# Performance work log

Hardware: AMD Instinct MI355X
Metric: run time of the kernel (lower is better)

Reference implementation:

```python
import jax, jax.numpy as jnp
import numpy as np

N_NODES = 100000


def _gcn_conv(x, W, b, src, dst, n_nodes):
    # PyG GCNConv: linear transform, then symmetric-normalized sum aggregation.
    h = x @ W  # [N, out]
    deg = jax.ops.segment_sum(jnp.ones_like(dst, dtype=h.dtype), dst, num_segments=n_nodes)
    dis = jnp.where(deg > 0, jax.lax.rsqrt(jnp.maximum(deg, 1.0)), 0.0)  # deg^-1/2
    norm = dis[src] * dis[dst]  # [E]
    msg = h[src] * norm[:, None]  # gather + scale
    out = jax.ops.segment_sum(msg, dst, num_segments=n_nodes)  # scatter-add at dst
    return out + b


def setup_inputs() -> dict:
    key = jax.random.key(0)
    k1, k2, k3, k4, k5, k6 = jax.random.split(key, 6)
    F_IN, HID, OUT = 128, 16, 2
    E = 3200000
    x = jax.random.normal(k1, (N_NODES, F_IN), dtype=jnp.float32)
    edge_index = jax.random.randint(k2, (2, E), 0, N_NODES, dtype=jnp.int64)
    W1 = jax.random.normal(k3, (F_IN, HID), dtype=jnp.float32) * (1.0 / np.sqrt(F_IN))
    b1 = jnp.zeros((HID,), dtype=jnp.float32)
    W2 = jax.random.normal(k4, (HID, OUT), dtype=jnp.float32) * (1.0 / np.sqrt(HID))
    b2 = jnp.zeros((OUT,), dtype=jnp.float32)
    return {"x": x, "edge_index": edge_index, "W1": W1, "b1": b1, "W2": W2, "b2": b2}


def reference(x, edge_index, W1, b1, W2, b2):
    n = x.shape[0]
    # add self-loops (PyG default add_self_loops=True, same edges for both layers)
    loops = jnp.arange(n, dtype=edge_index.dtype)
    src = jnp.concatenate([edge_index[0], loops])
    dst = jnp.concatenate([edge_index[1], loops])
    h = _gcn_conv(x, W1, b1, src, dst, n)
    h = jax.nn.relu(h)
    h = _gcn_conv(h, W2, b2, src, dst, n)
    return jax.nn.log_softmax(h, axis=1)
```

## Files before the change

### kernel.cpp

```cpp
#include <hip/hip_runtime.h>
#include <math.h>

#define FIN 128
#define HID 16
#define CH 8192
#define BSH 7
#define BNODES 128
#define LSH 25
#define SRCM 0x1FFFFFFu
#define SORTCAP 8192
#define BCAP 5120


__device__ __forceinline__ float bf2f(unsigned int bits16) {
    return __uint_as_float(bits16 << 16);
}
__device__ __forceinline__ unsigned short f2bf(float f) {
    unsigned int u = __float_as_uint(f);
    return (unsigned short)((u + 0x7FFFu + ((u >> 16) & 1u)) >> 16);
}

__device__ __forceinline__ int blockScan1024(int v, int* w16) {
    int lane = threadIdx.x & 63, wid = threadIdx.x >> 6;
#pragma unroll
    for (int off = 1; off < 64; off <<= 1) {
        int u = __shfl_up(v, off, 64);
        if (lane >= off) v += u;
    }
    if (lane == 63) w16[wid] = v;
    __syncthreads();
    if (wid == 0) {
        int w = (lane < 16) ? w16[lane] : 0;
#pragma unroll
        for (int off = 1; off < 16; off <<= 1) {
            int u = __shfl_up(w, off, 64);
            if (lane >= off) w += u;
        }
        if (lane < 16) w16[lane] = w;
    }
    __syncthreads();
    return v + ((wid > 0) ? w16[wid - 1] : 0);
}

__global__ void k_detect(const unsigned int* __restrict__ ew, int* __restrict__ flag) {
    __shared__ int nz;
    if (threadIdx.x == 0) nz = 0;
    __syncthreads();
    if (ew[2 * threadIdx.x + 1] != 0u) nz = 1;
    __syncthreads();
    if (threadIdx.x == 0) *flag = (nz == 0) ? 1 : 0;
}

__global__ __launch_bounds__(1024) void k_scatC(
    const void* __restrict__ ei, const int* __restrict__ flag,
    unsigned int* __restrict__ rec, int* __restrict__ runstart,
    int E, int NB) {
    __shared__ int h[1024];
    __shared__ int cur[1024];
    __shared__ int w16[16];
    __shared__ unsigned int outr[CH];
    int c = blockIdx.x, t = threadIdx.x;
    int e0 = c * CH;
    int ecnt = min(CH, E - e0);
    bool f = (*flag != 0);
    h[t] = 0;
    __syncthreads();
    for (int i = t; i < ecnt; i += 1024) {
        int d = f ? (int)((const long long*)ei)[E + e0 + i] : ((const int*)ei)[E + e0 + i];
        atomicAdd(&h[d >> BSH], 1);
    }
    __syncthreads();
    int v = h[t];
    int incl = blockScan1024(v, w16);
    int excl = incl - v;
    if (t < NB) {
        cur[t] = excl;
        runstart[(size_t)c * (NB + 1) + t] = excl;
    }
    if (t == 0) runstart[(size_t)c * (NB + 1) + NB] = ecnt;
    __syncthreads();
    for (int i = t; i < ecnt; i += 1024) {
        int ss, d;
        if (f) { const long long* p = (const long long*)ei; ss = (int)p[e0 + i]; d = (int)p[E + e0 + i]; }
        else   { const int* p = (const int*)ei;             ss = p[e0 + i];      d = p[E + e0 + i]; }
        int pos = atomicAdd(&cur[d >> BSH], 1);
        outr[pos] = ((unsigned int)(d & (BNODES - 1)) << LSH) | (unsigned int)ss;
    }
    __syncthreads();
    for (int i = t; i < ecnt; i += 1024)
        rec[e0 + i] = outr[i];
}

__global__ __launch_bounds__(1024) void k_sort2F(
    const unsigned int* __restrict__ rec, const int* __restrict__ runstart,
    unsigned int* __restrict__ rec2, int* __restrict__ row_ptr,
    int* __restrict__ cnt, int NB, int NC, int n) {
    __shared__ unsigned int stg[SORTCAP];
    __shared__ int w16[16];
    __shared__ int offA[512], lenA[512], baseA[512];
    __shared__ int h[BNODES], hs[BNODES], curq[BNODES];
    __shared__ int Ltot;
    int b = blockIdx.x, t = threadIdx.x;
    int l = 0, sbase = 0;
    if (t < NC) {
        const int* rs = runstart + (size_t)t * (NB + 1);
        int a = rs[b];
        l = rs[b + 1] - a;
        sbase = t * CH + a;
    }
    int incl = blockScan1024(l, w16);
    if (t < NC) { offA[t] = incl - l; lenA[t] = l; baseA[t] = sbase; }
    if (t < BNODES) h[t] = 0;
    if (t == 1023) Ltot = incl;
    __syncthreads();
    int L = min(Ltot, SORTCAP);
    int grp = t >> 4, lane16 = t & 15;
    for (int c = grp; c < NC; c += 64) {
        int off = offA[c], len = lenA[c], sb = baseA[c];
        for (int j = lane16; j < len; j += 16) {
            if (off + j < SORTCAP) {
                unsigned int r = rec[sb + j];
                stg[off + j] = r;
                atomicAdd(&h[r >> LSH], 1);
            }
        }
    }
    __syncthreads();
    int hv = (t < BNODES) ? h[t] : 0;
    if (t < BNODES) hs[t] = hv;
    __syncthreads();
    for (int off = 1; off < BNODES; off <<= 1) {
        int u = (t < BNODES && t >= off) ? hs[t - off] : 0;
        __syncthreads();
        if (t < BNODES) hs[t] += u;
        __syncthreads();
    }
    int bb = b * BCAP;
    if (t < BNODES) {
        int excl = hs[t] - hv;
        curq[t] = excl;
        int node = (b << BSH) + t;
        if (node < n) { row_ptr[node] = bb + excl; cnt[node] = hv; }
    }
    __syncthreads();
    for (int j = t; j < L; j += 1024) {
        unsigned int r = stg[j];
        int pos = atomicAdd(&curq[r >> LSH], 1);
        if (pos < BCAP) rec2[bb + pos] = r & SRCM;
    }
}

__global__ __launch_bounds__(256) void k_gemm1(
    const float* __restrict__ x, const float* __restrict__ W1,
    const int* __restrict__ cnt, unsigned short* __restrict__ g1b, int n) {
    __shared__ float sW[FIN][HID];
    for (int t = threadIdx.x; t < FIN * HID; t += 256) sW[t / HID][t % HID] = W1[t];
    __syncthreads();
    int i = blockIdx.x * 256 + threadIdx.x;
    if (i >= n) return;
    const float4* xr = (const float4*)(x + (size_t)i * FIN);
    float acc[HID];
#pragma unroll
    for (int c = 0; c < HID; ++c) acc[c] = 0.f;
    for (int k4 = 0; k4 < FIN / 4; ++k4) {
        float4 v = xr[k4];
#pragma unroll
        for (int c = 0; c < HID; ++c)
            acc[c] += v.x * sW[4*k4][c] + v.y * sW[4*k4+1][c]
                    + v.z * sW[4*k4+2][c] + v.w * sW[4*k4+3][c];
    }
    float di = rsqrtf((float)cnt[i] + 1.0f);
    unsigned int pk[8];
#pragma unroll
    for (int q = 0; q < 8; ++q) {
        unsigned int lo = f2bf(acc[2*q] * di);
        unsigned int hi = f2bf(acc[2*q+1] * di);
        pk[q] = lo | (hi << 16);
    }
    uint4* rp = (uint4*)(g1b + (size_t)i * HID);
    uint4 w0 = {pk[0], pk[1], pk[2], pk[3]};
    uint4 w1 = {pk[4], pk[5], pk[6], pk[7]};
    rp[0] = w0; rp[1] = w1;
}

__global__ __launch_bounds__(256) void k_agg1F(
    const int* __restrict__ row_ptr, const int* __restrict__ cnt,
    const unsigned int* __restrict__ rec2, const unsigned short* __restrict__ g1b,
    const float* __restrict__ b1, const float* __restrict__ W2,
    float* __restrict__ g2, int n) {
    int tid = blockIdx.x * 256 + threadIdx.x;
    int node = tid >> 2, q = tid & 3;
    if (node >= n) return;
    int r0 = row_ptr[node], r1 = r0 + cnt[node];
    const uint2* gp = (const uint2*)g1b;
    float a0 = 0.f, a1 = 0.f, a2 = 0.f, a3 = 0.f;
    int j = r0;
    for (; j + 3 < r1; j += 4) {
        unsigned int s0 = rec2[j], s1 = rec2[j+1], s2 = rec2[j+2], s3 = rec2[j+3];
        uint2 u0 = gp[(size_t)s0 * 4 + q];
        uint2 u1 = gp[(size_t)s1 * 4 + q];
        uint2 u2 = gp[(size_t)s2 * 4 + q];
        uint2 u3 = gp[(size_t)s3 * 4 + q];
        a0 += bf2f(u0.x & 0xFFFFu); a1 += bf2f(u0.x >> 16);
        a2 += bf2f(u0.y & 0xFFFFu); a3 += bf2f(u0.y >> 16);
        a0 += bf2f(u1.x & 0xFFFFu); a1 += bf2f(u1.x >> 16);
        a2 += bf2f(u1.y & 0xFFFFu); a3 += bf2f(u1.y >> 16);
        a0 += bf2f(u2.x & 0xFFFFu); a1 += bf2f(u2.x >> 16);
        a2 += bf2f(u2.y & 0xFFFFu); a3 += bf2f(u2.y >> 16);
        a0 += bf2f(u3.x & 0xFFFFu); a1 += bf2f(u3.x >> 16);
        a2 += bf2f(u3.y & 0xFFFFu); a3 += bf2f(u3.y >> 16);
    }
    for (; j < r1; ++j) {
        uint2 u = gp[(size_t)rec2[j] * 4 + q];
        a0 += bf2f(u.x & 0xFFFFu); a1 += bf2f(u.x >> 16);
        a2 += bf2f(u.y & 0xFFFFu); a3 += bf2f(u.y >> 16);
    }
    uint2 us = gp[(size_t)node * 4 + q];
    a0 += bf2f(us.x & 0xFFFFu); a1 += bf2f(us.x >> 16);
    a2 += bf2f(us.y & 0xFFFFu); a3 += bf2f(us.y >> 16);
    float di = rsqrtf((float)(r1 - r0) + 1.0f);
    int c4 = q << 2;
    float av[4] = {a0, a1, a2, a3};
    float h0 = 0.f, h1 = 0.f;
#pragma unroll
    for (int k = 0; k < 4; ++k) {
        int ch = c4 + k;
        float r = fmaxf(av[k] * di + b1[ch], 0.f);
        h0 += r * W2[ch * 2 + 0];
        h1 += r * W2[ch * 2 + 1];
    }
    h0 += __shfl_xor(h0, 1); h0 += __shfl_xor(h0, 2);
    h1 += __shfl_xor(h1, 1); h1 += __shfl_xor(h1, 2);
    if (q == 0) {
        float2 g; g.x = h0 * di; g.y = h1 * di;
        *(float2*)(g2 + 2 * (size_t)node) = g;
    }
}

__global__ __launch_bounds__(256) void k_aggB(
    const int* __restrict__ row_ptr, const int* __restrict__ cnt,
    const unsigned int* __restrict__ rec2, const float* __restrict__ g2,
    const float* __restrict__ b2, float* __restrict__ out, int n) {
    int tid = blockIdx.x * 256 + threadIdx.x;
    int node = tid >> 1, c = tid & 1;
    if (node >= n) return;
    int r0 = row_ptr[node], r1 = r0 + cnt[node];
    float a0 = 0.f, a1 = 0.f, a2 = 0.f, a3 = 0.f;
    int j = r0;
    for (; j + 3 < r1; j += 4) {
        unsigned int s0 = rec2[j], s1 = rec2[j+1], s2 = rec2[j+2], s3 = rec2[j+3];
        a0 += g2[2 * (size_t)s0 + c];
        a1 += g2[2 * (size_t)s1 + c];
        a2 += g2[2 * (size_t)s2 + c];
        a3 += g2[2 * (size_t)s3 + c];
    }
    for (; j < r1; ++j) a0 += g2[2 * (size_t)rec2[j] + c];
    float acc = (a0 + a1) + (a2 + a3);
    acc += g2[2 * (size_t)node + c];
    float di = rsqrtf((float)(r1 - r0) + 1.0f);
    float z  = acc * di + b2[c];
    float zo = __shfl_xor(z, 1);
    float mx = fmaxf(z, zo);
    float l  = mx + logf(expf(z - mx) + expf(zo - mx));
    out[2 * (size_t)node + c] = z - l;
}

extern "C" void kernel_launch(void* const* d_in, const int* in_sizes, int n_in,
                              void* d_out, int out_size, void* d_ws, size_t ws_size,
                              hipStream_t stream) {
    const float* x  = (const float*)d_in[0];
    const void*  ei = d_in[1];
    const float* W1 = (const float*)d_in[2];
    const float* b1 = (const float*)d_in[3];
    const float* W2 = (const float*)d_in[4];
    const float* b2 = (const float*)d_in[5];
    float* out = (float*)d_out;

    const int N = in_sizes[0] / FIN;
    const int E = in_sizes[1] / 2;

    const int NB = (N + BNODES - 1) >> BSH;
    const int NC = (E + CH - 1) / CH;

    char* w = (char*)d_ws;
    auto carve = [&](size_t bytes) { char* p = w; w += (bytes + 255) / 256 * 256; return p; };
    int*            flag     = (int*)carve(256);
    int*            runstart = (int*)carve((size_t)NC * (NB + 1) * 4);
    unsigned int*   rec      = (unsigned int*)carve((size_t)E * 4);
    unsigned int*   rec2     = (unsigned int*)carve((size_t)NB * BCAP * 4);
    int*            row_ptr  = (int*)carve((size_t)N * 4);
    int*            cnt      = (int*)carve((size_t)N * 4);
    unsigned short* g1b      = (unsigned short*)carve((size_t)N * HID * 2);
    float*          g2       = (float*)carve((size_t)N * 2 * 4);

    const int nbN = (N + 255) / 256;

    k_detect<<<1, 128, 0, stream>>>((const unsigned int*)ei, flag);
    k_scatC<<<NC, 1024, 0, stream>>>(ei, flag, rec, runstart, E, NB);
    k_sort2F<<<NB, 1024, 0, stream>>>(rec, runstart, rec2, row_ptr, cnt, NB, NC, N);
    k_gemm1<<<nbN, 256, 0, stream>>>(x, W1, cnt, g1b, N);
    k_agg1F<<<(N * 4 + 255) / 256, 256, 0, stream>>>(row_ptr, cnt, rec2, g1b, b1, W2, g2, N);
    k_aggB<<<(N * 2 + 255) / 256, 256, 0, stream>>>(row_ptr, cnt, rec2, g2, b2, out, N);
}
```

Measured before the change: 210.2 us.

## Fuse dtype detection, register-cache edges, nontemporal streams, widen aggregation threads

The separate dtype-detect kernel is folded into the scatter kernel. The scatter kernel now loads each edge's src and dst once into registers and reuses them, where it previously read the edge list twice. Streaming buffers use nontemporal loads and stores so they do not pollute the cache. The layer-1 aggregation moves from 4 to 2 threads per node with 16-byte gathers, and layer 2 uses one thread per node with 8-way unrolled float2 gathers. The changes cut launches, global reads and shuffles, but use more registers per thread and leave fewer threads to hide gather latency.

```diff
diff --git a/kernel.cpp b/kernel.cpp
--- a/kernel.cpp
+++ b/kernel.cpp
@@ -42,32 +42,41 @@
     return v + ((wid > 0) ? w16[wid - 1] : 0);
 }
 
-__global__ void k_detect(const unsigned int* __restrict__ ew, int* __restrict__ flag) {
-    __shared__ int nz;
-    if (threadIdx.x == 0) nz = 0;
-    __syncthreads();
-    if (ew[2 * threadIdx.x + 1] != 0u) nz = 1;
-    __syncthreads();
-    if (threadIdx.x == 0) *flag = (nz == 0) ? 1 : 0;
-}
-
 __global__ __launch_bounds__(1024) void k_scatC(
-    const void* __restrict__ ei, const int* __restrict__ flag,
-    unsigned int* __restrict__ rec, int* __restrict__ runstart,
-    int E, int NB) {
+    const void* __restrict__ ei, unsigned int* __restrict__ rec,
+    int* __restrict__ runstart, int E, int NB) {
     __shared__ int h[1024];
     __shared__ int cur[1024];
     __shared__ int w16[16];
+    __shared__ int s_f;
     __shared__ unsigned int outr[CH];
     int c = blockIdx.x, t = threadIdx.x;
     int e0 = c * CH;
     int ecnt = min(CH, E - e0);
-    bool f = (*flag != 0);
+    if (t == 0) s_f = 0;
     h[t] = 0;
     __syncthreads();
-    for (int i = t; i < ecnt; i += 1024) {
-        int d = f ? (int)((const long long*)ei)[E + e0 + i] : ((const int*)ei)[E + e0 + i];
-        atomicAdd(&h[d >> BSH], 1);
+    if (t < 128 && ((const unsigned int*)ei)[2 * t + 1] != 0u) s_f = 1;
+    __syncthreads();
+    bool f = (s_f == 0);
+    int sreg[CH / 1024], dreg[CH / 1024];
+    int nit = (ecnt + 1023 - t) >> 10;
+#pragma unroll
+    for (int k = 0; k < CH / 1024; ++k) {
+        int i = t + k * 1024;
+        if (i < ecnt) {
+            int idx = e0 + i;
+            if (f) {
+                const long long* p = (const long long*)ei;
+                sreg[k] = (int)__builtin_nontemporal_load(p + idx);
+                dreg[k] = (int)__builtin_nontemporal_load(p + E + idx);
+            } else {
+                const int* p = (const int*)ei;
+                sreg[k] = __builtin_nontemporal_load(p + idx);
+                dreg[k] = __builtin_nontemporal_load(p + E + idx);
+            }
+            atomicAdd(&h[dreg[k] >> BSH], 1);
+        }
     }
     __syncthreads();
     int v = h[t];
@@ -79,16 +88,18 @@
     }
     if (t == 0) runstart[(size_t)c * (NB + 1) + NB] = ecnt;
     __syncthreads();
-    for (int i = t; i < ecnt; i += 1024) {
-        int ss, d;
-        if (f) { const long long* p = (const long long*)ei; ss = (int)p[e0 + i]; d = (int)p[E + e0 + i]; }
-        else   { const int* p = (const int*)ei;             ss = p[e0 + i];      d = p[E + e0 + i]; }
-        int pos = atomicAdd(&cur[d >> BSH], 1);
-        outr[pos] = ((unsigned int)(d & (BNODES - 1)) << LSH) | (unsigned int)ss;
+#pragma unroll
+    for (int k = 0; k < CH / 1024; ++k) {
+        int i = t + k * 1024;
+        if (i < ecnt) {
+            int pos = atomicAdd(&cur[dreg[k] >> BSH], 1);
+            outr[pos] = ((unsigned int)(dreg[k] & (BNODES - 1)) << LSH) | (unsigned int)sreg[k];
+        }
     }
     __syncthreads();
     for (int i = t; i < ecnt; i += 1024)
-        rec[e0 + i] = outr[i];
+        __builtin_nontemporal_store(outr[i], &rec[e0 + i]);
+    (void)nit;
 }
 
 __global__ __launch_bounds__(1024) void k_sort2F(
@@ -119,7 +130,7 @@
         int off = offA[c], len = lenA[c], sb = baseA[c];
         for (int j = lane16; j < len; j += 16) {
             if (off + j < SORTCAP) {
-                unsigned int r = rec[sb + j];
+                unsigned int r = __builtin_nontemporal_load(&rec[sb + j]);
                 stg[off + j] = r;
                 atomicAdd(&h[r >> LSH], 1);
             }
@@ -146,7 +157,8 @@
     for (int j = t; j < L; j += 1024) {
         unsigned int r = stg[j];
         int pos = atomicAdd(&curq[r >> LSH], 1);
-        if (pos < BCAP) rec2[bb + pos] = r & SRCM;
+        if (pos < BCAP)
+            __builtin_nontemporal_store(r & SRCM, &rec2[bb + pos]);
     }
 }
 
@@ -189,48 +201,66 @@
     const float* __restrict__ b1, const float* __restrict__ W2,
     float* __restrict__ g2, int n) {
     int tid = blockIdx.x * 256 + threadIdx.x;
-    int node = tid >> 2, q = tid & 3;
+    int node = tid >> 1, q = tid & 1;
     if (node >= n) return;
-    int r0 = row_ptr[node], r1 = r0 + cnt[node];
-    const uint2* gp = (const uint2*)g1b;
-    float a0 = 0.f, a1 = 0.f, a2 = 0.f, a3 = 0.f;
+    int r0 = row_ptr[node], deg = cnt[node], r1 = r0 + deg;
+    const uint4* gp = (const uint4*)g1b;
+    float a[8];
+#pragma unroll
+    for (int k = 0; k < 8; ++k) a[k] = 0.f;
     int j = r0;
     for (; j + 3 < r1; j += 4) {
-        unsigned int s0 = rec2[j], s1 = rec2[j+1], s2 = rec2[j+2], s3 = rec2[j+3];
-        uint2 u0 = gp[(size_t)s0 * 4 + q];
-        uint2 u1 = gp[(size_t)s1 * 4 + q];
-        uint2 u2 = gp[(size_t)s2 * 4 + q];
-        uint2 u3 = gp[(size_t)s3 * 4 + q];
-        a0 += bf2f(u0.x & 0xFFFFu); a1 += bf2f(u0.x >> 16);
-        a2 += bf2f(u0.y & 0xFFFFu); a3 += bf2f(u0.y >> 16);
-        a0 += bf2f(u1.x & 0xFFFFu); a1 += bf2f(u1.x >> 16);
-        a2 += bf2f(u1.y & 0xFFFFu); a3 += bf2f(u1.y >> 16);
-        a0 += bf2f(u2.x & 0xFFFFu); a1 += bf2f(u2.x >> 16);
-        a2 += bf2f(u2.y & 0xFFFFu); a3 += bf2f(u2.y >> 16);
-        a0 += bf2f(u3.x & 0xFFFFu); a1 += bf2f(u3.x >> 16);
-        a2 += bf2f(u3.y & 0xFFFFu); a3 += bf2f(u3.y >> 16);
+        unsigned int s0 = __builtin_nontemporal_load(&rec2[j]);
+        unsigned int s1 = __builtin_nontemporal_load(&rec2[j+1]);
+        unsigned int s2 = __builtin_nontemporal_load(&rec2[j+2]);
+        unsigned int s3 = __builtin_nontemporal_load(&rec2[j+3]);
+        uint4 u0 = gp[(size_t)s0 * 2 + q];
+        uint4 u1 = gp[(size_t)s1 * 2 + q];
+        uint4 u2 = gp[(size_t)s2 * 2 + q];
+        uint4 u3 = gp[(size_t)s3 * 2 + q];
+#pragma unroll
+        for (int k = 0; k < 1; ++k) { }
+        a[0] += bf2f(u0.x & 0xFFFFu); a[1] += bf2f(u0.x >> 16);
+        a[2] += bf2f(u0.y & 0xFFFFu); a[3] += bf2f(u0.y >> 16);
+        a[4] += bf2f(u0.z & 0xFFFFu); a[5] += bf2f(u0.z >> 16);
+        a[6] += bf2f(u0.w & 0xFFFFu); a[7] += bf2f(u0.w >> 16);
+        a[0] += bf2f(u1.x & 0xFFFFu); a[1] += bf2f(u1.x >> 16);
+        a[2] += bf2f(u1.y & 0xFFFFu); a[3] += bf2f(u1.y >> 16);
+        a[4] += bf2f(u1.z & 0xFFFFu); a[5] += bf2f(u1.z >> 16);
+        a[6] += bf2f(u1.w & 0xFFFFu); a[7] += bf2f(u1.w >> 16);
+        a[0] += bf2f(u2.x & 0xFFFFu); a[1] += bf2f(u2.x >> 16);
+        a[2] += bf2f(u2.y & 0xFFFFu); a[3] += bf2f(u2.y >> 16);
+        a[4] += bf2f(u2.z & 0xFFFFu); a[5] += bf2f(u2.z >> 16);
+        a[6] += bf2f(u2.w & 0xFFFFu); a[7] += bf2f(u2.w >> 16);
+        a[0] += bf2f(u3.x & 0xFFFFu); a[1] += bf2f(u3.x >> 16);
+        a[2] += bf2f(u3.y & 0xFFFFu); a[3] += bf2f(u3.y >> 16);
+        a[4] += bf2f(u3.z & 0xFFFFu); a[5] += bf2f(u3.z >> 16);
+        a[6] += bf2f(u3.w & 0xFFFFu); a[7] += bf2f(u3.w >> 16);
     }
     for (; j < r1; ++j) {
-        uint2 u = gp[(size_t)rec2[j] * 4 + q];
-        a0 += bf2f(u.x & 0xFFFFu); a1 += bf2f(u.x >> 16);
-        a2 += bf2f(u.y & 0xFFFFu); a3 += bf2f(u.y >> 16);
-    }
-    uint2 us = gp[(size_t)node * 4 + q];
-    a0 += bf2f(us.x & 0xFFFFu); a1 += bf2f(us.x >> 16);
-    a2 += bf2f(us.y & 0xFFFFu); a3 += bf2f(us.y >> 16);
-    float di = rsqrtf((float)(r1 - r0) + 1.0f);
-    int c4 = q << 2;
-    float av[4] = {a0, a1, a2, a3};
+        unsigned int s = __builtin_nontemporal_load(&rec2[j]);
+        uint4 u = gp[(size_t)s * 2 + q];
+        a[0] += bf2f(u.x & 0xFFFFu); a[1] += bf2f(u.x >> 16);
+        a[2] += bf2f(u.y & 0xFFFFu); a[3] += bf2f(u.y >> 16);
+        a[4] += bf2f(u.z & 0xFFFFu); a[5] += bf2f(u.z >> 16);
+        a[6] += bf2f(u.w & 0xFFFFu); a[7] += bf2f(u.w >> 16);
+    }
+    uint4 us = gp[(size_t)node * 2 + q];
+    a[0] += bf2f(us.x & 0xFFFFu); a[1] += bf2f(us.x >> 16);
+    a[2] += bf2f(us.y & 0xFFFFu); a[3] += bf2f(us.y >> 16);
+    a[4] += bf2f(us.z & 0xFFFFu); a[5] += bf2f(us.z >> 16);
+    a[6] += bf2f(us.w & 0xFFFFu); a[7] += bf2f(us.w >> 16);
+    float di = rsqrtf((float)deg + 1.0f);
     float h0 = 0.f, h1 = 0.f;
 #pragma unroll
-    for (int k = 0; k < 4; ++k) {
-        int ch = c4 + k;
-        float r = fmaxf(av[k] * di + b1[ch], 0.f);
+    for (int k = 0; k < 8; ++k) {
+        int ch = q * 8 + k;
+        float r = fmaxf(a[k] * di + b1[ch], 0.f);
         h0 += r * W2[ch * 2 + 0];
         h1 += r * W2[ch * 2 + 1];
     }
-    h0 += __shfl_xor(h0, 1); h0 += __shfl_xor(h0, 2);
-    h1 += __shfl_xor(h1, 1); h1 += __shfl_xor(h1, 2);
+    h0 += __shfl_xor(h0, 1);
+    h1 += __shfl_xor(h1, 1);
     if (q == 0) {
         float2 g; g.x = h0 * di; g.y = h1 * di;
         *(float2*)(g2 + 2 * (size_t)node) = g;
@@ -241,28 +271,39 @@
     const int* __restrict__ row_ptr, const int* __restrict__ cnt,
     const unsigned int* __restrict__ rec2, const float* __restrict__ g2,
     const float* __restrict__ b2, float* __restrict__ out, int n) {
-    int tid = blockIdx.x * 256 + threadIdx.x;
-    int node = tid >> 1, c = tid & 1;
+    int node = blockIdx.x * 256 + threadIdx.x;
     if (node >= n) return;
-    int r0 = row_ptr[node], r1 = r0 + cnt[node];
-    float a0 = 0.f, a1 = 0.f, a2 = 0.f, a3 = 0.f;
+    int r0 = row_ptr[node], deg = cnt[node], r1 = r0 + deg;
+    const float2* gp = (const float2*)g2;
+    float x0 = 0.f, y0 = 0.f, x1 = 0.f, y1 = 0.f;
     int j = r0;
-    for (; j + 3 < r1; j += 4) {
-        unsigned int s0 = rec2[j], s1 = rec2[j+1], s2 = rec2[j+2], s3 = rec2[j+3];
-        a0 += g2[2 * (size_t)s0 + c];
-        a1 += g2[2 * (size_t)s1 + c];
-        a2 += g2[2 * (size_t)s2 + c];
-        a3 += g2[2 * (size_t)s3 + c];
-    }
-    for (; j < r1; ++j) a0 += g2[2 * (size_t)rec2[j] + c];
-    float acc = (a0 + a1) + (a2 + a3);
-    acc += g2[2 * (size_t)node + c];
-    float di = rsqrtf((float)(r1 - r0) + 1.0f);
-    float z  = acc * di + b2[c];
-    float zo = __shfl_xor(z, 1);
-    float mx = fmaxf(z, zo);
-    float l  = mx + logf(expf(z - mx) + expf(zo - mx));
-    out[2 * (size_t)node + c] = z - l;
+    for (; j + 7 < r1; j += 8) {
+        unsigned int s[8];
+#pragma unroll
+        for (int k = 0; k < 8; ++k) s[k] = __builtin_nontemporal_load(&rec2[j + k]);
+        float2 v[8];
+#pragma unroll
+        for (int k = 0; k < 8; ++k) v[k] = gp[s[k]];
+#pragma unroll
+        for (int k = 0; k < 8; k += 2) {
+            x0 += v[k].x;     y0 += v[k].y;
+            x1 += v[k + 1].x; y1 += v[k + 1].y;
+        }
+    }
+    for (; j < r1; ++j) {
+        float2 v = gp[__builtin_nontemporal_load(&rec2[j])];
+        x0 += v.x; y0 += v.y;
+    }
+    float2 vs = gp[node];
+    float z0 = x0 + x1 + vs.x;
+    float z1 = y0 + y1 + vs.y;
+    float di = rsqrtf((float)deg + 1.0f);
+    z0 = z0 * di + b2[0];
+    z1 = z1 * di + b2[1];
+    float m = fmaxf(z0, z1);
+    float l = m + logf(expf(z0 - m) + expf(z1 - m));
+    out[2 * (size_t)node]     = z0 - l;
+    out[2 * (size_t)node + 1] = z1 - l;
 }
 
 extern "C" void kernel_launch(void* const* d_in, const int* in_sizes, int n_in,
@@ -284,7 +325,6 @@
 
     char* w = (char*)d_ws;
     auto carve = [&](size_t bytes) { char* p = w; w += (bytes + 255) / 256 * 256; return p; };
-    int*            flag     = (int*)carve(256);
     int*            runstart = (int*)carve((size_t)NC * (NB + 1) * 4);
     unsigned int*   rec      = (unsigned int*)carve((size_t)E * 4);
     unsigned int*   rec2     = (unsigned int*)carve((size_t)NB * BCAP * 4);
@@ -295,10 +335,9 @@
 
     const int nbN = (N + 255) / 256;
 
-    k_detect<<<1, 128, 0, stream>>>((const unsigned int*)ei, flag);
-    k_scatC<<<NC, 1024, 0, stream>>>(ei, flag, rec, runstart, E, NB);
+    k_scatC<<<NC, 1024, 0, stream>>>(ei, rec, runstart, E, NB);
     k_sort2F<<<NB, 1024, 0, stream>>>(rec, runstart, rec2, row_ptr, cnt, NB, NC, N);
     k_gemm1<<<nbN, 256, 0, stream>>>(x, W1, cnt, g1b, N);
-    k_agg1F<<<(N * 4 + 255) / 256, 256, 0, stream>>>(row_ptr, cnt, rec2, g1b, b1, W2, g2, N);
-    k_aggB<<<(N * 2 + 255) / 256, 256, 0, stream>>>(row_ptr, cnt, rec2, g2, b2, out, N);
-}
+    k_agg1F<<<(N * 2 + 255) / 256, 256, 0, stream>>>(row_ptr, cnt, rec2, g1b, b1, W2, g2, N);
+    k_aggB<<<nbN, 256, 0, stream>>>(row_ptr, cnt, rec2, g2, b2, out, N);
+}
```

After: 307.6 us. +46.4%, slower.
